# Performance work log

Hardware: AMD Instinct MI355X
Metric: run time of the kernel (lower is better)

Reference implementation:

```python
import jax, jax.numpy as jnp
import numpy as np
import math

# ---- dims ----
B, N, IN_DIM = 4, 512, 128
D, H, DH = 256, 8, 32          # embed_dim, heads, dim_head
L = 8                           # performer depth
M = int(DH * math.log(DH))      # 110 FAVOR+ random features (performer_pytorch default)
HID = 256                       # lstm hidden
FF = 4 * D
EPS_K = 1e-4                    # kernel feature eps
EPS_D = 1e-6                    # denominator eps


def setup_inputs() -> dict:
    key = jax.random.key(0)
    ks = iter(jax.random.split(key, 40))
    def nrm(shape, s=0.02):
        return jax.random.normal(next(ks), shape, dtype=jnp.float32) * s
    z = lambda shape: jnp.zeros(shape, jnp.float32)
    o = lambda shape: jnp.ones(shape, jnp.float32)
    return {
        "x": jax.random.normal(next(ks), (B, N, IN_DIM), dtype=jnp.float32),
        # input projection
        "Win_w": nrm((D, IN_DIM)), "Win_b": z((D,)),
        # performer layers (stacked over L)
        "ln1_w": o((L, D)), "ln1_b": z((L, D)),
        "Wq": nrm((L, D, D)), "bq": z((L, D)),
        "Wk": nrm((L, D, D)), "bk": z((L, D)),
        "Wv": nrm((L, D, D)), "bv": z((L, D)),
        "Wo": nrm((L, D, D)), "bo": z((L, D)),
        "proj": jax.random.normal(next(ks), (L, M, DH), dtype=jnp.float32),  # FAVOR+ projections
        "ln2_w": o((L, D)), "ln2_b": z((L, D)),
        "Wff1": nrm((L, FF, D)), "bff1": z((L, FF)),
        "Wff2": nrm((L, D, FF)), "bff2": z((L, D)),
        # BiLSTM: layer0 input D, layers1-2 input 2*HID; [dir] / [layer,dir] stacks
        "Wih0": nrm((2, 4 * HID, D)), "Whh0": nrm((2, 4 * HID, HID)), "b0": z((2, 2, 4 * HID)),
        "Wih12": nrm((2, 2, 4 * HID, 2 * HID)), "Whh12": nrm((2, 2, 4 * HID, HID)), "b12": z((2, 2, 2, 4 * HID)),
        # final head
        "fc_w": nrm((1, 2 * HID)), "fc_b": z((1,)),
    }


def layer_norm(x, w, b):
    mu = jnp.mean(x, -1, keepdims=True)
    var = jnp.mean((x - mu) ** 2, -1, keepdims=True)
    return (x - mu) * jax.lax.rsqrt(var + 1e-5) * w + b


def softmax_features(x, proj, is_query):
    # FAVOR+ positive softmax-kernel features. x:[b,h,n,dh], proj:[m,dh]
    xd = x * (DH ** -0.25)
    dd = jnp.einsum('bhnd,md->bhnm', xd, proj)
    diag = 0.5 * jnp.sum(xd * xd, -1)[..., None]            # [b,h,n,1]
    if is_query:
        stab = jnp.max(dd, axis=-1, keepdims=True)
    else:
        stab = jnp.max(dd, axis=(-2, -1), keepdims=True)
    return (M ** -0.5) * (jnp.exp(dd - diag - stab) + EPS_K)


def causal_linear_attention(qp, kp, v):
    # qp,kp:[b,h,n,m], v:[b,h,n,dv] -> [b,h,n,dv]; cumulative-sum causal form
    k_cum = jnp.cumsum(kp, axis=2)
    d_inv = 1.0 / (jnp.einsum('bhnm,bhnm->bhn', qp, k_cum) + EPS_D)
    ctx = jnp.cumsum(jnp.einsum('bhnm,bhnd->bhnmd', kp, v), axis=2)
    return jnp.einsum('bhnmd,bhnm,bhn->bhnd', ctx, qp, d_inv)


def performer_block(x, p):
    (lw1, lb1, wq, bq_, wk, bk_, wv, bv_, wo, bo_, pr, lw2, lb2, w1, b1, w2, b2) = p
    b, n = x.shape[0], x.shape[1]
    y = layer_norm(x, lw1, lb1)
    sh = lambda t: t.reshape(b, n, H, DH).transpose(0, 2, 1, 3)
    q = sh(y @ wq.T + bq_)
    k = sh(y @ wk.T + bk_)
    v = sh(y @ wv.T + bv_)
    qp = softmax_features(q, pr, True)
    kp = softmax_features(k, pr, False)
    o = causal_linear_attention(qp, kp, v)
    o = o.transpose(0, 2, 1, 3).reshape(b, n, D)
    x = x + o @ wo.T + bo_
    y = layer_norm(x, lw2, lb2)
    x = x + jax.nn.gelu(y @ w1.T + b1, approximate=False) @ w2.T + b2
    return x, None


def lstm_dir(x, wih, whh, b, reverse):
    # x:[B,N,in] -> hs:[B,N,HID]; torch gate order i,f,g,o
    xs = jnp.flip(x, 1) if reverse else x
    gi = xs.transpose(1, 0, 2) @ wih.T + b                  # [N,B,4H] precomputed input part
    def step(carry, g_in):
        h, c = carry
        g = g_in + h @ whh.T
        i, f, gg, oo = jnp.split(g, 4, axis=-1)
        c = jax.nn.sigmoid(f) * c + jax.nn.sigmoid(i) * jnp.tanh(gg)
        h = jax.nn.sigmoid(oo) * jnp.tanh(c)
        return (h, c), h
    h0 = jnp.zeros((x.shape[0], HID), x.dtype)
    _, hs = jax.lax.scan(step, (h0, h0), gi)
    hs = hs.transpose(1, 0, 2)
    return jnp.flip(hs, 1) if reverse else hs


def bilstm_layer(x, wih, whh, b):
    fwd = lstm_dir(x, wih[0], whh[0], b[0, 0] + b[0, 1], False)
    bwd = lstm_dir(x, wih[1], whh[1], b[1, 0] + b[1, 1], True)
    return jnp.concatenate([fwd, bwd], -1)


def reference(x, Win_w, Win_b, ln1_w, ln1_b, Wq, bq, Wk, bk, Wv, bv, Wo, bo, proj,
              ln2_w, ln2_b, Wff1, bff1, Wff2, bff2,
              Wih0, Whh0, b0, Wih12, Whh12, b12, fc_w, fc_b):
    h = x @ Win_w.T + Win_b
    params = (ln1_w, ln1_b, Wq, bq, Wk, bk, Wv, bv, Wo, bo, proj, ln2_w, ln2_b, Wff1, bff1, Wff2, bff2)
    h, _ = jax.lax.scan(performer_block, h, params)       # 8 performer layers
    # dropout is identity at eval
    h = bilstm_layer(h, Wih0, Whh0, b0)
    h = bilstm_layer(h, Wih12[0], Whh12[0], b12[0])
    h = bilstm_layer(h, Wih12[1], Whh12[1], b12[1])
    return h[:, -1, :] @ fc_w.T + fc_b                    # [B,1]
```

## Files before the change

### kernel.cpp

```cpp
#include <hip/hip_runtime.h>
#include <math.h>

#define B_    4
#define N_    512
#define D_    256
#define H_    8
#define DH_   32
#define M_    110
#define MP_   112
#define FF_   1024
#define HID_  256
#define ROWS_ 2048
#define CHUNK 32
#define NCH   16

#define OFF_H      0u
#define OFF_Y      524288u
#define OFF_Q      1048576u
#define OFF_K      1572864u
#define OFF_V      2097152u
#define OFF_O      2621440u
#define OFF_FF     3145728u
#define OFF_QP     5242880u
#define OFF_KP     7077888u
#define OFF_S      8912896u
#define OFF_MB     9437184u
#define OFF_P      10747904u
#define OFF_KSUM   12582912u
#define OFF_PK     12640256u
#define OFF_DIAG   12697600u
#define OFF_KMAX   12713984u

#define SCALE_X 0.42044820762685725f
#define SCALE_M 0.09534625892455924f

__device__ __forceinline__ float sigmoidf_(float x){ return 1.0f/(1.0f+expf(-x)); }
__device__ __forceinline__ float geluf_(float x){ return 0.5f*x*(1.0f+erff(x*0.70710678118654752f)); }
__device__ __forceinline__ unsigned encf_(float x){ unsigned u=__float_as_uint(x); return (u&0x80000000u)?~u:(u|0x80000000u); }
__device__ __forceinline__ float decf_(unsigned u){ return (u&0x80000000u)?__uint_as_float(u&0x7fffffffu):__uint_as_float(~u); }

typedef unsigned u32x4_ __attribute__((ext_vector_type(4)));

__device__ __forceinline__ u32x4_ ld4_far_(const unsigned* p){
  u32x4_ v;
  asm volatile("global_load_dwordx4 %0, %1, off sc0 sc1\n\ts_waitcnt vmcnt(0)"
               : "=v"(v) : "v"(p));
  return v;
}

__global__ __launch_bounds__(256) void gemm_k(
    const float* __restrict__ A, const float* __restrict__ W,
    const float* __restrict__ b1, const float* __restrict__ b2,
    const float* __restrict__ R, float* __restrict__ C,
    int M, int N, int K, int act)
{
  __shared__ float As[16][72];
  __shared__ float Ws[16][72];
  const int tid = threadIdx.x;
  const int tx = tid & 15, ty = tid >> 4;
  const int i0 = blockIdx.y * 64, j0 = blockIdx.x * 64;
  const int lr = tid >> 2, lc = (tid & 3) << 2;
  float acc[4][4] = {};
  for (int k0 = 0; k0 < K; k0 += 16) {
    float4 a4 = *(const float4*)(A + (size_t)(i0 + lr) * K + k0 + lc);
    float4 w4 = *(const float4*)(W + (size_t)(j0 + lr) * K + k0 + lc);
    __syncthreads();
    As[lc+0][lr]=a4.x; As[lc+1][lr]=a4.y; As[lc+2][lr]=a4.z; As[lc+3][lr]=a4.w;
    Ws[lc+0][lr]=w4.x; Ws[lc+1][lr]=w4.y; Ws[lc+2][lr]=w4.z; Ws[lc+3][lr]=w4.w;
    __syncthreads();
    #pragma unroll
    for (int kk = 0; kk < 16; kk++) {
      float4 av = *(const float4*)&As[kk][ty*4];
      float4 wv = *(const float4*)&Ws[kk][tx*4];
      acc[0][0] += av.x*wv.x; acc[0][1] += av.x*wv.y; acc[0][2] += av.x*wv.z; acc[0][3] += av.x*wv.w;
      acc[1][0] += av.y*wv.x; acc[1][1] += av.y*wv.y; acc[1][2] += av.y*wv.z; acc[1][3] += av.y*wv.w;
      acc[2][0] += av.z*wv.x; acc[2][1] += av.z*wv.y; acc[2][2] += av.z*wv.z; acc[2][3] += av.z*wv.w;
      acc[3][0] += av.w*wv.x; acc[3][1] += av.w*wv.y; acc[3][2] += av.w*wv.z; acc[3][3] += av.w*wv.w;
    }
  }
  #pragma unroll
  for (int ii = 0; ii < 4; ii++) {
    int gi_ = i0 + ty*4 + ii;
    #pragma unroll
    for (int jj = 0; jj < 4; jj++) {
      int gj = j0 + tx*4 + jj;
      float v = acc[ii][jj];
      if (b1) v += b1[gj];
      if (b2) v += b2[gj];
      if (act) v = geluf_(v);
      if (R) v += R[(size_t)gi_ * N + gj];
      C[(size_t)gi_ * N + gj] = v;
    }
  }
}

__global__ __launch_bounds__(256) void gemm3_k(
    const float* __restrict__ A,
    const float* __restrict__ W0, const float* __restrict__ W1, const float* __restrict__ W2,
    const float* __restrict__ c0_, const float* __restrict__ c1_, const float* __restrict__ c2_,
    float* __restrict__ O0, float* __restrict__ O1, float* __restrict__ O2)
{
  const int which = blockIdx.x >> 2;
  const float* W  = which == 0 ? W0 : which == 1 ? W1 : W2;
  const float* bb = which == 0 ? c0_ : which == 1 ? c1_ : c2_;
  float* C        = which == 0 ? O0 : which == 1 ? O1 : O2;
  __shared__ float As[16][72];
  __shared__ float Ws[16][72];
  const int tid = threadIdx.x;
  const int tx = tid & 15, ty = tid >> 4;
  const int i0 = blockIdx.y * 64, j0 = (blockIdx.x & 3) * 64;
  const int lr = tid >> 2, lc = (tid & 3) << 2;
  float acc[4][4] = {};
  for (int k0 = 0; k0 < 256; k0 += 16) {
    float4 a4 = *(const float4*)(A + (size_t)(i0 + lr) * 256 + k0 + lc);
    float4 w4 = *(const float4*)(W + (size_t)(j0 + lr) * 256 + k0 + lc);
    __syncthreads();
    As[lc+0][lr]=a4.x; As[lc+1][lr]=a4.y; As[lc+2][lr]=a4.z; As[lc+3][lr]=a4.w;
    Ws[lc+0][lr]=w4.x; Ws[lc+1][lr]=w4.y; Ws[lc+2][lr]=w4.z; Ws[lc+3][lr]=w4.w;
    __syncthreads();
    #pragma unroll
    for (int kk = 0; kk < 16; kk++) {
      float4 av = *(const float4*)&As[kk][ty*4];
      float4 wv = *(const float4*)&Ws[kk][tx*4];
      acc[0][0] += av.x*wv.x; acc[0][1] += av.x*wv.y; acc[0][2] += av.x*wv.z; acc[0][3] += av.x*wv.w;
      acc[1][0] += av.y*wv.x; acc[1][1] += av.y*wv.y; acc[1][2] += av.y*wv.z; acc[1][3] += av.y*wv.w;
      acc[2][0] += av.z*wv.x; acc[2][1] += av.z*wv.y; acc[2][2] += av.z*wv.z; acc[2][3] += av.z*wv.w;
      acc[3][0] += av.w*wv.x; acc[3][1] += av.w*wv.y; acc[3][2] += av.w*wv.z; acc[3][3] += av.w*wv.w;
    }
  }
  #pragma unroll
  for (int ii = 0; ii < 4; ii++) {
    int gi_ = i0 + ty*4 + ii;
    #pragma unroll
    for (int jj = 0; jj < 4; jj++) {
      int gj = j0 + tx*4 + jj;
      C[(size_t)gi_ * 256 + gj] = acc[ii][jj] + bb[gj];
    }
  }
}

__global__ __launch_bounds__(256) void gemmgi_k(
    const float* __restrict__ A, const float* __restrict__ W, const float* __restrict__ bvec,
    float* __restrict__ C, int K, int wGap, int bGap)
{
  const int dir = blockIdx.x >> 4;
  const float* Wd = W + (size_t)dir * wGap;
  const float* b1 = bvec + (size_t)dir * bGap;
  const float* b2 = b1 + 1024;
  float* Cd = C + (size_t)dir * 2097152;
  __shared__ float As[16][72];
  __shared__ float Ws[16][72];
  const int tid = threadIdx.x;
  const int tx = tid & 15, ty = tid >> 4;
  const int i0 = blockIdx.y * 64, j0 = (blockIdx.x & 15) * 64;
  const int lr = tid >> 2, lc = (tid & 3) << 2;
  float acc[4][4] = {};
  for (int k0 = 0; k0 < K; k0 += 16) {
    float4 a4 = *(const float4*)(A + (size_t)(i0 + lr) * K + k0 + lc);
    float4 w4 = *(const float4*)(Wd + (size_t)(j0 + lr) * K + k0 + lc);
    __syncthreads();
    As[lc+0][lr]=a4.x; As[lc+1][lr]=a4.y; As[lc+2][lr]=a4.z; As[lc+3][lr]=a4.w;
    Ws[lc+0][lr]=w4.x; Ws[lc+1][lr]=w4.y; Ws[lc+2][lr]=w4.z; Ws[lc+3][lr]=w4.w;
    __syncthreads();
    #pragma unroll
    for (int kk = 0; kk < 16; kk++) {
      float4 av = *(const float4*)&As[kk][ty*4];
      float4 wv = *(const float4*)&Ws[kk][tx*4];
      acc[0][0] += av.x*wv.x; acc[0][1] += av.x*wv.y; acc[0][2] += av.x*wv.z; acc[0][3] += av.x*wv.w;
      acc[1][0] += av.y*wv.x; acc[1][1] += av.y*wv.y; acc[1][2] += av.y*wv.z; acc[1][3] += av.y*wv.w;
      acc[2][0] += av.z*wv.x; acc[2][1] += av.z*wv.y; acc[2][2] += av.z*wv.z; acc[2][3] += av.z*wv.w;
      acc[3][0] += av.w*wv.x; acc[3][1] += av.w*wv.y; acc[3][2] += av.w*wv.z; acc[3][3] += av.w*wv.w;
    }
  }
  #pragma unroll
  for (int ii = 0; ii < 4; ii++) {
    int gi_ = i0 + ty*4 + ii;
    #pragma unroll
    for (int jj = 0; jj < 4; jj++) {
      int gj = j0 + tx*4 + jj;
      Cd[(size_t)gi_ * 1024 + gj] = acc[ii][jj] + b1[gj] + b2[gj];
    }
  }
}

__global__ __launch_bounds__(256) void ln_k(const float* __restrict__ x, const float* __restrict__ w,
                                            const float* __restrict__ b, float* __restrict__ y)
{
  const int row = blockIdx.x, t = threadIdx.x;
  float v = x[(size_t)row * 256 + t];
  float s = v;
  #pragma unroll
  for (int o = 32; o >= 1; o >>= 1) s += __shfl_xor(s, o, 64);
  __shared__ float w1_[4], w2_[4];
  const int wid = t >> 6, lane = t & 63;
  if (lane == 0) w1_[wid] = s;
  __syncthreads();
  float mu = (w1_[0] + w1_[1] + w1_[2] + w1_[3]) * (1.0f/256.0f);
  float d = v - mu;
  float s2 = d * d;
  #pragma unroll
  for (int o = 32; o >= 1; o >>= 1) s2 += __shfl_xor(s2, o, 64);
  if (lane == 0) w2_[wid] = s2;
  __syncthreads();
  float var = (w2_[0] + w2_[1] + w2_[2] + w2_[3]) * (1.0f/256.0f);
  y[(size_t)row * 256 + t] = d * (1.0f / sqrtf(var + 1e-5f)) * w[t] + b[t];
}

__global__ __launch_bounds__(256) void feat_k(const float* __restrict__ q, const float* __restrict__ kk,
                                              const float* __restrict__ proj,
                                              float* __restrict__ qp, float* __restrict__ kpraw,
                                              float* __restrict__ diagb, unsigned* __restrict__ kmax)
{
  const int isq = (blockIdx.x < 4096);
  const int bx = isq ? blockIdx.x : (blockIdx.x - 4096);
  const int wid = threadIdx.x >> 6, lane = threadIdx.x & 63;
  const int p = bx * 4 + wid;
  const int bh = p >> 9, n = p & 511;
  const int b = bh >> 3, h = bh & 7;
  __shared__ float xs[4][32];
  const float* xrow = (isq ? q : kk) + ((size_t)(b * N_ + n)) * D_ + h * DH_;
  if (lane < 32) xs[wid][lane] = xrow[lane] * SCALE_X;
  __syncthreads();
  float diag = 0.f;
  #pragma unroll
  for (int d = 0; d < 32; d++) { float xv = xs[wid][d]; diag += xv * xv; }
  diag *= 0.5f;
  const int m0 = lane, m1 = 64 + lane;
  float dd0 = 0.f, dd1 = -INFINITY;
  #pragma unroll
  for (int d = 0; d < 32; d++) dd0 += xs[wid][d] * proj[m0 * 32 + d];
  if (m1 < M_) {
    float a = 0.f;
    #pragma unroll
    for (int d = 0; d < 32; d++) a += xs[wid][d] * proj[m1 * 32 + d];
    dd1 = a;
  }
  float mx = fmaxf(dd0, dd1);
  #pragma unroll
  for (int o = 32; o >= 1; o >>= 1) mx = fmaxf(mx, __shfl_xor(mx, o, 64));
  if (isq) {
    float* out = qp + (size_t)p * MP_;
    out[m0] = SCALE_M * (expf(dd0 - diag - mx) + 1e-4f);
    if (m1 < M_)        out[m1] = SCALE_M * (expf(dd1 - diag - mx) + 1e-4f);
    else if (m1 < MP_)  out[m1] = 0.f;
  } else {
    float* out = kpraw + (size_t)p * MP_;
    out[m0] = dd0;
    if (m1 < M_) out[m1] = dd1;
    if (lane == 0) { diagb[p] = diag; atomicMax(kmax + bh, encf_(mx)); }
  }
}

__global__ __launch_bounds__(256) void csum_k(const float* __restrict__ kp, const float* __restrict__ v,
                                              const float* __restrict__ diagb, const unsigned* __restrict__ kmax,
                                              float* __restrict__ S, float* __restrict__ ksum)
{
  const int bh = blockIdx.x >> 4, c = blockIdx.x & 15;
  const int b = bh >> 3, h = bh & 7;
  __shared__ float kpc[CHUNK * MP_];
  __shared__ float vc[CHUNK][DH_];
  const float* kpbase = kp + ((size_t)bh * N_ + c * CHUNK) * MP_;
  const float kmx = decf_(kmax[bh]);
  const int r0 = bh * N_ + c * CHUNK;
  for (int f = threadIdx.x; f < CHUNK * MP_; f += 256) {
    int i = f / MP_, m = f - i * MP_;
    float raw = kpbase[f];
    float val = 0.f;
    if (m < M_) val = SCALE_M * (expf(raw - diagb[r0 + i] - kmx) + 1e-4f);
    kpc[f] = val;
  }
  for (int f = threadIdx.x; f < CHUNK * DH_; f += 256) {
    int i = f >> 5, d = f & 31;
    vc[i][d] = v[((size_t)(b * N_ + c * CHUNK + i)) * D_ + h * DH_ + d];
  }
  __syncthreads();
  const int d = threadIdx.x & 31, mg = threadIdx.x >> 5;
  float Sa[14] = {};
  for (int i = 0; i < CHUNK; i++) {
    float vv = vc[i][d];
    #pragma unroll
    for (int j = 0; j < 14; j++) Sa[j] += kpc[i * MP_ + mg * 14 + j] * vv;
  }
  float* Sout = S + (((size_t)blockIdx.x) * MP_ + mg * 14) * DH_ + d;
  #pragma unroll
  for (int j = 0; j < 14; j++) Sout[(size_t)j * DH_] = Sa[j];
  if (threadIdx.x < MP_) {
    float s = 0.f;
    for (int i = 0; i < CHUNK; i++) s += kpc[i * MP_ + threadIdx.x];
    ksum[(size_t)blockIdx.x * MP_ + threadIdx.x] = s;
  }
}

__global__ __launch_bounds__(256) void cpref_k(const float* __restrict__ S, const float* __restrict__ ksum,
                                               float* __restrict__ P, float* __restrict__ pk)
{
  const int bh = blockIdx.x;
  const int d = threadIdx.x & 31, mg = threadIdx.x >> 5;
  float run[14] = {};
  for (int c = 0; c < NCH; c++) {
    size_t base = (((size_t)(bh * NCH + c)) * MP_ + mg * 14) * DH_ + d;
    #pragma unroll
    for (int j = 0; j < 14; j++) { P[base + (size_t)j * DH_] = run[j]; run[j] += S[base + (size_t)j * DH_]; }
  }
  if (threadIdx.x < MP_) {
    float r = 0.f;
    for (int c = 0; c < NCH; c++) {
      size_t o = (size_t)(bh * NCH + c) * MP_ + threadIdx.x;
      pk[o] = r; r += ksum[o];
    }
  }
}

__global__ __launch_bounds__(256, 1) void attn_k(const float* __restrict__ qp, const float* __restrict__ kp,
                                                 const float* __restrict__ v, const float* __restrict__ P,
                                                 const float* __restrict__ pk,
                                                 const float* __restrict__ diagb, const unsigned* __restrict__ kmax,
                                                 float* __restrict__ o)
{
  const int bh = blockIdx.x >> 4, c = blockIdx.x & 15;
  const int b = bh >> 3, h = bh & 7;
  __shared__ float qpc[CHUNK * 113];
  __shared__ float kpc[CHUNK * 113];
  __shared__ float vc[CHUNK][DH_];
  __shared__ float Pl[MP_ * DH_];
  __shared__ float pkl[MP_];
  __shared__ float Al[CHUNK * 33];
  __shared__ float den[CHUNK];
  const int t = threadIdx.x;
  const float* qbase = qp + ((size_t)bh * N_ + c * CHUNK) * MP_;
  const float* kbase = kp + ((size_t)bh * N_ + c * CHUNK) * MP_;
  const float kmx = decf_(kmax[bh]);
  const int r0 = bh * N_ + c * CHUNK;
  for (int f = t; f < CHUNK * MP_; f += 256) {
    int i = f / MP_, m = f - i * MP_;
    qpc[i * 113 + m] = qbase[f];
    float raw = kbase[f];
    float val = 0.f;
    if (m < M_) val = SCALE_M * (expf(raw - diagb[r0 + i] - kmx) + 1e-4f);
    kpc[i * 113 + m] = val;
  }
  for (int f = t; f < CHUNK * DH_; f += 256) {
    int i = f >> 5, d = f & 31;
    vc[i][d] = v[((size_t)(b * N_ + c * CHUNK + i)) * D_ + h * DH_ + d];
  }
  for (int f = t; f < MP_ * DH_; f += 256) Pl[f] = P[((size_t)blockIdx.x) * MP_ * DH_ + f];
  if (t < MP_) pkl[t] = pk[(size_t)blockIdx.x * MP_ + t];
  __syncthreads();
  {
    const int ti = t >> 4, tj = t & 15;
    float a00 = 0.f, a01 = 0.f, a10 = 0.f, a11 = 0.f;
    for (int m = 0; m < MP_; m++) {
      float q0 = qpc[(ti*2+0)*113 + m], q1 = qpc[(ti*2+1)*113 + m];
      float k0 = kpc[(tj*2+0)*113 + m], k1 = kpc[(tj*2+1)*113 + m];
      a00 += q0*k0; a01 += q0*k1; a10 += q1*k0; a11 += q1*k1;
    }
    const int i0_ = ti*2, j0_ = tj*2;
    Al[(i0_  )*33 + j0_  ] = (j0_   <= i0_  ) ? a00 : 0.f;
    Al[(i0_  )*33 + j0_+1] = (j0_+1 <= i0_  ) ? a01 : 0.f;
    Al[(i0_+1)*33 + j0_  ] = (j0_   <= i0_+1) ? a10 : 0.f;
    Al[(i0_+1)*33 + j0_+1] = (j0_+1 <= i0_+1) ? a11 : 0.f;
  }
  __syncthreads();
  if (t < CHUNK) {
    const int i = t; float s = 0.f;
    for (int m = 0; m < MP_; m++) s += qpc[i*113 + m] * pkl[m];
    for (int j = 0; j <= i; j++) s += Al[i*33 + j];
    den[i] = 1.0f / (s + 1e-6f);
  }
  __syncthreads();
  {
    const int d = t & 31, ig = t >> 5;
    float Pd[MP_];
    #pragma unroll
    for (int m = 0; m < MP_; m++) Pd[m] = Pl[m * DH_ + d];
    float vd[CHUNK];
    #pragma unroll
    for (int j = 0; j < CHUNK; j++) vd[j] = vc[j][d];
    for (int r = 0; r < 4; r++) {
      const int i = ig * 4 + r;
      float acc = 0.f;
      #pragma unroll
      for (int m = 0; m < MP_; m++) acc += qpc[i*113 + m] * Pd[m];
      #pragma unroll
      for (int j = 0; j < CHUNK; j++) acc += Al[i*33 + j] * vd[j];
      o[((size_t)(b * N_ + c * CHUNK + i)) * D_ + h * DH_ + d] = acc * den[i];
    }
  }
}

__global__ __launch_bounds__(256, 1) void rec_k(
    const float* __restrict__ gi, const float* __restrict__ whh,
    float* __restrict__ hs, float* __restrict__ hx)
{
  const int bid = blockIdx.x;
  if ((bid & 7) > 1) return;
  const int dir = bid & 7;
  const int s = bid >> 3;
  if (s >= 16) return;
  const int t = threadIdx.x;

  __shared__ __align__(16) float h_sh[4][256];
  __shared__ __align__(16) float red[64 * 33];

  __builtin_amdgcn_fence(__ATOMIC_ACQUIRE, "agent");

  const float* giD = gi + (size_t)dir * 2097152;
  const float* whD = whh + (size_t)dir * 262144;
  float* hxD = hx + (size_t)dir * 524288;

  const int rg = t & 31, kq = t >> 5;
  float4 w4[2][8];
  #pragma unroll
  for (int rr = 0; rr < 2; rr++) {
    const int rho = rg * 2 + rr;
    const int grow = (rho >> 4) * 256 + s * 16 + (rho & 15);
    const float4* src = (const float4*)(whD + (size_t)grow * 256 + kq * 32);
    #pragma unroll
    for (int q = 0; q < 8; q++) w4[rr][q] = src[q];
  }

  const int j = t & 15, bb = t >> 4;
  const float* pgi0 = giD + (size_t)bb * 524288 + (size_t)(s * 16 + j);

  ((float4*)h_sh)[t] = make_float4(0.f, 0.f, 0.f, 0.f);
  float c0 = 0.f;
  __syncthreads();

  int n = dir ? 511 : 0;
  float gnext[4];
  if (t < 64) {
    #pragma unroll
    for (int g = 0; g < 4; g++) gnext[g] = pgi0[(size_t)n * 1024 + g * 256];
  }

  for (int step = 0; step < 512; step++) {
    const int n2 = dir ? (510 - step) : (step + 1);
    float gcur[4];
    if (t < 64) {
      #pragma unroll
      for (int g = 0; g < 4; g++) gcur[g] = gnext[g];
      if (step < 511) {
        #pragma unroll
        for (int g = 0; g < 4; g++) gnext[g] = pgi0[(size_t)n2 * 1024 + g * 256];
      }
    }

    float acc[2][4] = {};
    #pragma unroll
    for (int q = 0; q < 8; q++) {
      float4 h0 = *(const float4*)&h_sh[0][kq * 32 + q * 4];
      float4 h1 = *(const float4*)&h_sh[1][kq * 32 + q * 4];
      float4 h2 = *(const float4*)&h_sh[2][kq * 32 + q * 4];
      float4 h3 = *(const float4*)&h_sh[3][kq * 32 + q * 4];
      #pragma unroll
      for (int rr = 0; rr < 2; rr++) {
        float4 w = w4[rr][q];
        acc[rr][0] += w.x*h0.x + w.y*h0.y + w.z*h0.z + w.w*h0.w;
        acc[rr][1] += w.x*h1.x + w.y*h1.y + w.z*h1.z + w.w*h1.w;
        acc[rr][2] += w.x*h2.x + w.y*h2.y + w.z*h2.z + w.w*h2.w;
        acc[rr][3] += w.x*h3.x + w.y*h3.y + w.z*h3.z + w.w*h3.w;
      }
    }
    #pragma unroll
    for (int rr = 0; rr < 2; rr++)
      #pragma unroll
      for (int b = 0; b < 4; b++)
        red[(rg * 2 + rr) * 33 + b * 8 + kq] = acc[rr][b];
    __syncthreads();

    if (t < 64) {
      float pre[4];
      #pragma unroll
      for (int g = 0; g < 4; g++) {
        const float* rp = &red[(g * 16 + j) * 33 + bb * 8];
        float sum = gcur[g];
        #pragma unroll
        for (int q = 0; q < 8; q++) sum += rp[q];
        pre[g] = sum;
      }
      c0 = sigmoidf_(pre[1]) * c0 + sigmoidf_(pre[0]) * tanhf(pre[2]);
      const float hv = sigmoidf_(pre[3]) * tanhf(c0);
      if (step < 511) {
        __hip_atomic_store(hxD + (size_t)step * 1024 + bb * 256 + s * 16 + j, hv,
                           __ATOMIC_RELAXED, __HIP_MEMORY_SCOPE_AGENT);
      }
      hs[(size_t)(bb * 512 + n) * 512 + dir * 256 + s * 16 + j] = hv;
    }

    if (step < 511) {
      const unsigned* pp = (const unsigned*)(hxD + (size_t)step * 1024) + t * 4;
      u32x4_ v = ld4_far_(pp);
      while (v.x == 0xFFFFFFFFu || v.y == 0xFFFFFFFFu ||
             v.z == 0xFFFFFFFFu || v.w == 0xFFFFFFFFu) {
        v = ld4_far_(pp);
      }
      float4 hv4;
      hv4.x = __uint_as_float(v.x); hv4.y = __uint_as_float(v.y);
      hv4.z = __uint_as_float(v.z); hv4.w = __uint_as_float(v.w);
      ((float4*)h_sh)[t] = hv4;
      __syncthreads();
    }
    n = n2;
  }
}

__global__ __launch_bounds__(256) void fc_k(const float* __restrict__ hs, const float* __restrict__ fw,
                                            const float* __restrict__ fb, float* __restrict__ out)
{
  const int t = threadIdx.x;
  float p[4] = {};
  for (int j = t; j < 512; j += 256) {
    const float w = fw[j];
    #pragma unroll
    for (int b = 0; b < 4; b++) p[b] += hs[(size_t)(b * 512 + 511) * 512 + j] * w;
  }
  #pragma unroll
  for (int b = 0; b < 4; b++)
    #pragma unroll
    for (int o = 32; o >= 1; o >>= 1) p[b] += __shfl_xor(p[b], o, 64);
  __shared__ float r4[4][4];
  const int wid = t >> 6, lane = t & 63;
  if (lane == 0) {
    #pragma unroll
    for (int b = 0; b < 4; b++) r4[b][wid] = p[b];
  }
  __syncthreads();
  if (t == 0) {
    #pragma unroll
    for (int b = 0; b < 4; b++) out[b] = r4[b][0] + r4[b][1] + r4[b][2] + r4[b][3] + fb[0];
  }
}

extern "C" void kernel_launch(void* const* d_in, const int* in_sizes, int n_in,
                              void* d_out, int out_size, void* d_ws, size_t ws_size,
                              hipStream_t stream) {
  (void)in_sizes; (void)n_in; (void)out_size; (void)ws_size;
  const float* x     = (const float*)d_in[0];
  const float* Win_w = (const float*)d_in[1];
  const float* Win_b = (const float*)d_in[2];
  const float* ln1w  = (const float*)d_in[3];
  const float* ln1b  = (const float*)d_in[4];
  const float* Wq    = (const float*)d_in[5];
  const float* bq    = (const float*)d_in[6];
  const float* Wk    = (const float*)d_in[7];
  const float* bk    = (const float*)d_in[8];
  const float* Wv    = (const float*)d_in[9];
  const float* bv    = (const float*)d_in[10];
  const float* Wo    = (const float*)d_in[11];
  const float* bo    = (const float*)d_in[12];
  const float* proj  = (const float*)d_in[13];
  const float* ln2w  = (const float*)d_in[14];
  const float* ln2b  = (const float*)d_in[15];
  const float* Wff1  = (const float*)d_in[16];
  const float* bff1  = (const float*)d_in[17];
  const float* Wff2  = (const float*)d_in[18];
  const float* bff2  = (const float*)d_in[19];
  const float* Wih0  = (const float*)d_in[20];
  const float* Whh0  = (const float*)d_in[21];
  const float* b0    = (const float*)d_in[22];
  const float* Wih12 = (const float*)d_in[23];
  const float* Whh12 = (const float*)d_in[24];
  const float* b12   = (const float*)d_in[25];
  const float* fcw   = (const float*)d_in[26];
  const float* fcb   = (const float*)d_in[27];

  float* ws = (float*)d_ws;
  float* H   = ws + OFF_H;
  float* Y   = ws + OFF_Y;
  float* Q   = ws + OFF_Q;
  float* Kb  = ws + OFF_K;
  float* V   = ws + OFF_V;
  float* O   = ws + OFF_O;
  float* FFb = ws + OFF_FF;
  float* QP  = ws + OFF_QP;
  float* KP  = ws + OFF_KP;
  float* S   = ws + OFF_S;
  float* P   = ws + OFF_P;
  float* KS  = ws + OFF_KSUM;
  float* PK  = ws + OFF_PK;
  float* DG  = ws + OFF_DIAG;
  unsigned* KMAX = (unsigned*)(ws + OFF_KMAX);
  float* GI  = ws + OFF_QP;
  float* MA  = ws + OFF_MB;
  float* BLa = ws + OFF_FF;
  float* BLb = ws + OFF_FF + 1048576;

  const dim3 blk(256);
  const dim3 g256(4, 32);
  const dim3 g768(12, 32);
  const dim3 g1024(16, 32);
  const dim3 g2048(32, 32);

  gemm_k<<<g256, blk, 0, stream>>>(x, Win_w, Win_b, nullptr, nullptr, H, ROWS_, 256, 128, 0);

  for (int l = 0; l < 8; l++) {
    const float* prj = proj + (size_t)l * 3520;
    ln_k<<<ROWS_, blk, 0, stream>>>(H, ln1w + l*256, ln1b + l*256, Y);
    gemm3_k<<<g768, blk, 0, stream>>>(Y, Wq + (size_t)l*65536, Wk + (size_t)l*65536, Wv + (size_t)l*65536,
                                      bq + l*256, bk + l*256, bv + l*256, Q, Kb, V);
    (void)hipMemsetAsync(KMAX, 0, 32 * sizeof(unsigned), stream);
    feat_k<<<8192, blk, 0, stream>>>(Q, Kb, prj, QP, KP, DG, KMAX);
    csum_k<<<512, blk, 0, stream>>>(KP, V, DG, KMAX, S, KS);
    cpref_k<<<32, blk, 0, stream>>>(S, KS, P, PK);
    attn_k<<<512, blk, 0, stream>>>(QP, KP, V, P, PK, DG, KMAX, O);
    gemm_k<<<g256, blk, 0, stream>>>(O, Wo + (size_t)l*65536, bo + l*256, nullptr, H, H, ROWS_, 256, 256, 0);
    ln_k<<<ROWS_, blk, 0, stream>>>(H, ln2w + l*256, ln2b + l*256, Y);
    gemm_k<<<g1024, blk, 0, stream>>>(Y, Wff1 + (size_t)l*262144, bff1 + l*1024, nullptr, nullptr, FFb, ROWS_, 1024, 256, 1);
    gemm_k<<<g256, blk, 0, stream>>>(FFb, Wff2 + (size_t)l*262144, bff2 + l*256, nullptr, H, H, ROWS_, 256, 1024, 0);
  }

  (void)hipMemsetAsync(MA, 0xFF, 3145728u * sizeof(float), stream);

  gemmgi_k<<<g2048, blk, 0, stream>>>(H, Wih0, b0, GI, 256, 262144, 2048);
  rec_k<<<128, blk, 0, stream>>>(GI, Whh0, BLa, MA);

  gemmgi_k<<<g2048, blk, 0, stream>>>(BLa, Wih12, b12, GI, 512, 524288, 2048);
  rec_k<<<128, blk, 0, stream>>>(GI, Whh12, BLb, MA + 1048576);

  gemmgi_k<<<g2048, blk, 0, stream>>>(BLb, Wih12 + 1048576, b12 + 4096, GI, 512, 524288, 2048);
  rec_k<<<128, blk, 0, stream>>>(GI, Whh12 + 524288, BLa, MA + 2097152);

  fc_k<<<1, blk, 0, stream>>>(BLa, fcw, fcb, (float*)d_out);
}
```

Baseline: 6.807 ms.

## Use 32x32 GEMM tiles for narrow outputs, prefetch tiles, fold prefix into attention

Adds a 32x32-tile GEMM with 2x2 register blocking for the 256-wide output GEMMs (input projection, Wo, FF2) and the QKV GEMM, giving four times as many blocks to fill the GPU. All tiled GEMMs now load the next K-slice into registers while the current shared-memory tile is being computed. The separate chunk-prefix kernel is removed: each attention block sums the preceding chunk states itself, which repeats some global reads. The per-layer KMAX memset is replaced by a single memset over per-layer slices, saving one launch per layer.

```diff
diff --git a/kernel.cpp b/kernel.cpp
--- a/kernel.cpp
+++ b/kernel.cpp
@@ -48,6 +48,111 @@
   return v;
 }
 
+__global__ __launch_bounds__(256) void gemms_k(
+    const float* __restrict__ A, const float* __restrict__ W,
+    const float* __restrict__ b1, const float* __restrict__ b2,
+    const float* __restrict__ R, float* __restrict__ C,
+    int M, int N, int K, int act)
+{
+  __shared__ float As[16][36];
+  __shared__ float Ws[16][36];
+  const int tid = threadIdx.x;
+  const int tx = tid & 15, ty = tid >> 4;
+  const int i0 = blockIdx.y * 32, j0 = blockIdx.x * 32;
+  const int lr = tid >> 3, lc = (tid & 7) << 1;
+  const float* pA = A + (size_t)(i0 + lr) * K + lc;
+  const float* pW = W + (size_t)(j0 + lr) * K + lc;
+  float a00=0.f, a01=0.f, a10=0.f, a11=0.f;
+  float2 a2 = *(const float2*)pA;
+  float2 w2 = *(const float2*)pW;
+  for (int k0 = 0; k0 < K; k0 += 16) {
+    __syncthreads();
+    As[lc+0][lr]=a2.x; As[lc+1][lr]=a2.y;
+    Ws[lc+0][lr]=w2.x; Ws[lc+1][lr]=w2.y;
+    float2 a2n = a2, w2n = w2;
+    if (k0 + 16 < K) {
+      a2n = *(const float2*)(pA + k0 + 16);
+      w2n = *(const float2*)(pW + k0 + 16);
+    }
+    __syncthreads();
+    #pragma unroll
+    for (int kk = 0; kk < 16; kk++) {
+      float2 av = *(const float2*)&As[kk][ty*2];
+      float2 wv = *(const float2*)&Ws[kk][tx*2];
+      a00 += av.x*wv.x; a01 += av.x*wv.y;
+      a10 += av.y*wv.x; a11 += av.y*wv.y;
+    }
+    a2 = a2n; w2 = w2n;
+  }
+  float accv[2][2] = {{a00,a01},{a10,a11}};
+  #pragma unroll
+  for (int ii = 0; ii < 2; ii++) {
+    int gi_ = i0 + ty*2 + ii;
+    #pragma unroll
+    for (int jj = 0; jj < 2; jj++) {
+      int gj = j0 + tx*2 + jj;
+      float v = accv[ii][jj];
+      if (b1) v += b1[gj];
+      if (b2) v += b2[gj];
+      if (act) v = geluf_(v);
+      if (R) v += R[(size_t)gi_ * N + gj];
+      C[(size_t)gi_ * N + gj] = v;
+    }
+  }
+}
+
+__global__ __launch_bounds__(256) void gemm3_k(
+    const float* __restrict__ A,
+    const float* __restrict__ W0, const float* __restrict__ W1, const float* __restrict__ W2,
+    const float* __restrict__ c0_, const float* __restrict__ c1_, const float* __restrict__ c2_,
+    float* __restrict__ O0, float* __restrict__ O1, float* __restrict__ O2)
+{
+  const int which = blockIdx.x >> 3;
+  const float* W  = which == 0 ? W0 : which == 1 ? W1 : W2;
+  const float* bb = which == 0 ? c0_ : which == 1 ? c1_ : c2_;
+  float* C        = which == 0 ? O0 : which == 1 ? O1 : O2;
+  __shared__ float As[16][36];
+  __shared__ float Ws[16][36];
+  const int tid = threadIdx.x;
+  const int tx = tid & 15, ty = tid >> 4;
+  const int i0 = blockIdx.y * 32, j0 = (blockIdx.x & 7) * 32;
+  const int lr = tid >> 3, lc = (tid & 7) << 1;
+  const float* pA = A + (size_t)(i0 + lr) * 256 + lc;
+  const float* pW = W + (size_t)(j0 + lr) * 256 + lc;
+  float a00=0.f, a01=0.f, a10=0.f, a11=0.f;
+  float2 a2 = *(const float2*)pA;
+  float2 w2 = *(const float2*)pW;
+  for (int k0 = 0; k0 < 256; k0 += 16) {
+    __syncthreads();
+    As[lc+0][lr]=a2.x; As[lc+1][lr]=a2.y;
+    Ws[lc+0][lr]=w2.x; Ws[lc+1][lr]=w2.y;
+    float2 a2n = a2, w2n = w2;
+    if (k0 + 16 < 256) {
+      a2n = *(const float2*)(pA + k0 + 16);
+      w2n = *(const float2*)(pW + k0 + 16);
+    }
+    __syncthreads();
+    #pragma unroll
+    for (int kk = 0; kk < 16; kk++) {
+      float2 av = *(const float2*)&As[kk][ty*2];
+      float2 wv = *(const float2*)&Ws[kk][tx*2];
+      a00 += av.x*wv.x; a01 += av.x*wv.y;
+      a10 += av.y*wv.x; a11 += av.y*wv.y;
+    }
+    a2 = a2n; w2 = w2n;
+  }
+  float accv[2][2] = {{a00,a01},{a10,a11}};
+  #pragma unroll
+  for (int ii = 0; ii < 2; ii++) {
+    int gi_ = i0 + ty*2 + ii;
+    #pragma unroll
+    for (int jj = 0; jj < 2; jj++) {
+      int gj = j0 + tx*2 + jj;
+      C[(size_t)gi_ * 256 + gj] = accv[ii][jj] + bb[gj];
+    }
+  }
+}
+
 __global__ __launch_bounds__(256) void gemm_k(
     const float* __restrict__ A, const float* __restrict__ W,
     const float* __restrict__ b1, const float* __restrict__ b2,
@@ -60,13 +165,20 @@
   const int tx = tid & 15, ty = tid >> 4;
   const int i0 = blockIdx.y * 64, j0 = blockIdx.x * 64;
   const int lr = tid >> 2, lc = (tid & 3) << 2;
+  const float* pA = A + (size_t)(i0 + lr) * K + lc;
+  const float* pW = W + (size_t)(j0 + lr) * K + lc;
   float acc[4][4] = {};
+  float4 a4 = *(const float4*)pA;
+  float4 w4 = *(const float4*)pW;
   for (int k0 = 0; k0 < K; k0 += 16) {
-    float4 a4 = *(const float4*)(A + (size_t)(i0 + lr) * K + k0 + lc);
-    float4 w4 = *(const float4*)(W + (size_t)(j0 + lr) * K + k0 + lc);
     __syncthreads();
     As[lc+0][lr]=a4.x; As[lc+1][lr]=a4.y; As[lc+2][lr]=a4.z; As[lc+3][lr]=a4.w;
     Ws[lc+0][lr]=w4.x; Ws[lc+1][lr]=w4.y; Ws[lc+2][lr]=w4.z; Ws[lc+3][lr]=w4.w;
+    float4 a4n = a4, w4n = w4;
+    if (k0 + 16 < K) {
+      a4n = *(const float4*)(pA + k0 + 16);
+      w4n = *(const float4*)(pW + k0 + 16);
+    }
     __syncthreads();
     #pragma unroll
     for (int kk = 0; kk < 16; kk++) {
@@ -77,6 +189,7 @@
       acc[2][0] += av.z*wv.x; acc[2][1] += av.z*wv.y; acc[2][2] += av.z*wv.z; acc[2][3] += av.z*wv.w;
       acc[3][0] += av.w*wv.x; acc[3][1] += av.w*wv.y; acc[3][2] += av.w*wv.z; acc[3][3] += av.w*wv.w;
     }
+    a4 = a4n; w4 = w4n;
   }
   #pragma unroll
   for (int ii = 0; ii < 4; ii++) {
@@ -90,51 +203,6 @@
       if (act) v = geluf_(v);
       if (R) v += R[(size_t)gi_ * N + gj];
       C[(size_t)gi_ * N + gj] = v;
-    }
-  }
-}
-
-__global__ __launch_bounds__(256) void gemm3_k(
-    const float* __restrict__ A,
-    const float* __restrict__ W0, const float* __restrict__ W1, const float* __restrict__ W2,
-    const float* __restrict__ c0_, const float* __restrict__ c1_, const float* __restrict__ c2_,
-    float* __restrict__ O0, float* __restrict__ O1, float* __restrict__ O2)
-{
-  const int which = blockIdx.x >> 2;
-  const float* W  = which == 0 ? W0 : which == 1 ? W1 : W2;
-  const float* bb = which == 0 ? c0_ : which == 1 ? c1_ : c2_;
-  float* C        = which == 0 ? O0 : which == 1 ? O1 : O2;
-  __shared__ float As[16][72];
-  __shared__ float Ws[16][72];
-  const int tid = threadIdx.x;
-  const int tx = tid & 15, ty = tid >> 4;
-  const int i0 = blockIdx.y * 64, j0 = (blockIdx.x & 3) * 64;
-  const int lr = tid >> 2, lc = (tid & 3) << 2;
-  float acc[4][4] = {};
-  for (int k0 = 0; k0 < 256; k0 += 16) {
-    float4 a4 = *(const float4*)(A + (size_t)(i0 + lr) * 256 + k0 + lc);
-    float4 w4 = *(const float4*)(W + (size_t)(j0 + lr) * 256 + k0 + lc);
-    __syncthreads();
-    As[lc+0][lr]=a4.x; As[lc+1][lr]=a4.y; As[lc+2][lr]=a4.z; As[lc+3][lr]=a4.w;
-    Ws[lc+0][lr]=w4.x; Ws[lc+1][lr]=w4.y; Ws[lc+2][lr]=w4.z; Ws[lc+3][lr]=w4.w;
-    __syncthreads();
-    #pragma unroll
-    for (int kk = 0; kk < 16; kk++) {
-      float4 av = *(const float4*)&As[kk][ty*4];
-      float4 wv = *(const float4*)&Ws[kk][tx*4];
-      acc[0][0] += av.x*wv.x; acc[0][1] += av.x*wv.y; acc[0][2] += av.x*wv.z; acc[0][3] += av.x*wv.w;
-      acc[1][0] += av.y*wv.x; acc[1][1] += av.y*wv.y; acc[1][2] += av.y*wv.z; acc[1][3] += av.y*wv.w;
-      acc[2][0] += av.z*wv.x; acc[2][1] += av.z*wv.y; acc[2][2] += av.z*wv.z; acc[2][3] += av.z*wv.w;
-      acc[3][0] += av.w*wv.x; acc[3][1] += av.w*wv.y; acc[3][2] += av.w*wv.z; acc[3][3] += av.w*wv.w;
-    }
-  }
-  #pragma unroll
-  for (int ii = 0; ii < 4; ii++) {
-    int gi_ = i0 + ty*4 + ii;
-    #pragma unroll
-    for (int jj = 0; jj < 4; jj++) {
-      int gj = j0 + tx*4 + jj;
-      C[(size_t)gi_ * 256 + gj] = acc[ii][jj] + bb[gj];
     }
   }
 }
@@ -154,13 +222,20 @@
   const int tx = tid & 15, ty = tid >> 4;
   const int i0 = blockIdx.y * 64, j0 = (blockIdx.x & 15) * 64;
   const int lr = tid >> 2, lc = (tid & 3) << 2;
+  const float* pA = A + (size_t)(i0 + lr) * K + lc;
+  const float* pW = Wd + (size_t)(j0 + lr) * K + lc;
   float acc[4][4] = {};
+  float4 a4 = *(const float4*)pA;
+  float4 w4 = *(const float4*)pW;
   for (int k0 = 0; k0 < K; k0 += 16) {
-    float4 a4 = *(const float4*)(A + (size_t)(i0 + lr) * K + k0 + lc);
-    float4 w4 = *(const float4*)(Wd + (size_t)(j0 + lr) * K + k0 + lc);
     __syncthreads();
     As[lc+0][lr]=a4.x; As[lc+1][lr]=a4.y; As[lc+2][lr]=a4.z; As[lc+3][lr]=a4.w;
     Ws[lc+0][lr]=w4.x; Ws[lc+1][lr]=w4.y; Ws[lc+2][lr]=w4.z; Ws[lc+3][lr]=w4.w;
+    float4 a4n = a4, w4n = w4;
+    if (k0 + 16 < K) {
+      a4n = *(const float4*)(pA + k0 + 16);
+      w4n = *(const float4*)(pW + k0 + 16);
+    }
     __syncthreads();
     #pragma unroll
     for (int kk = 0; kk < 16; kk++) {
@@ -171,6 +246,7 @@
       acc[2][0] += av.z*wv.x; acc[2][1] += av.z*wv.y; acc[2][2] += av.z*wv.z; acc[2][3] += av.z*wv.w;
       acc[3][0] += av.w*wv.x; acc[3][1] += av.w*wv.y; acc[3][2] += av.w*wv.z; acc[3][3] += av.w*wv.w;
     }
+    a4 = a4n; w4 = w4n;
   }
   #pragma unroll
   for (int ii = 0; ii < 4; ii++) {
@@ -291,29 +367,9 @@
   }
 }
 
-__global__ __launch_bounds__(256) void cpref_k(const float* __restrict__ S, const float* __restrict__ ksum,
-                                               float* __restrict__ P, float* __restrict__ pk)
-{
-  const int bh = blockIdx.x;
-  const int d = threadIdx.x & 31, mg = threadIdx.x >> 5;
-  float run[14] = {};
-  for (int c = 0; c < NCH; c++) {
-    size_t base = (((size_t)(bh * NCH + c)) * MP_ + mg * 14) * DH_ + d;
-    #pragma unroll
-    for (int j = 0; j < 14; j++) { P[base + (size_t)j * DH_] = run[j]; run[j] += S[base + (size_t)j * DH_]; }
-  }
-  if (threadIdx.x < MP_) {
-    float r = 0.f;
-    for (int c = 0; c < NCH; c++) {
-      size_t o = (size_t)(bh * NCH + c) * MP_ + threadIdx.x;
-      pk[o] = r; r += ksum[o];
-    }
-  }
-}
-
 __global__ __launch_bounds__(256, 1) void attn_k(const float* __restrict__ qp, const float* __restrict__ kp,
-                                                 const float* __restrict__ v, const float* __restrict__ P,
-                                                 const float* __restrict__ pk,
+                                                 const float* __restrict__ v,
+                                                 const float* __restrict__ S, const float* __restrict__ ksum,
                                                  const float* __restrict__ diagb, const unsigned* __restrict__ kmax,
                                                  float* __restrict__ o)
 {
@@ -343,8 +399,20 @@
     int i = f >> 5, d = f & 31;
     vc[i][d] = v[((size_t)(b * N_ + c * CHUNK + i)) * D_ + h * DH_ + d];
   }
-  for (int f = t; f < MP_ * DH_; f += 256) Pl[f] = P[((size_t)blockIdx.x) * MP_ * DH_ + f];
-  if (t < MP_) pkl[t] = pk[(size_t)blockIdx.x * MP_ + t];
+  {
+    const float* Sb = S + (size_t)(bh * NCH) * MP_ * DH_;
+    for (int f = t; f < MP_ * DH_; f += 256) {
+      float accp = 0.f;
+      for (int cc = 0; cc < c; cc++) accp += Sb[(size_t)cc * MP_ * DH_ + f];
+      Pl[f] = accp;
+    }
+    if (t < MP_) {
+      const float* Kb2 = ksum + (size_t)(bh * NCH) * MP_;
+      float r = 0.f;
+      for (int cc = 0; cc < c; cc++) r += Kb2[(size_t)cc * MP_ + t];
+      pkl[t] = r;
+    }
+  }
   __syncthreads();
   {
     const int ti = t >> 4, tj = t & 15;
@@ -575,9 +643,7 @@
   float* QP  = ws + OFF_QP;
   float* KP  = ws + OFF_KP;
   float* S   = ws + OFF_S;
-  float* P   = ws + OFF_P;
   float* KS  = ws + OFF_KSUM;
-  float* PK  = ws + OFF_PK;
   float* DG  = ws + OFF_DIAG;
   unsigned* KMAX = (unsigned*)(ws + OFF_KMAX);
   float* GI  = ws + OFF_QP;
@@ -586,38 +652,39 @@
   float* BLb = ws + OFF_FF + 1048576;
 
   const dim3 blk(256);
-  const dim3 g256(4, 32);
-  const dim3 g768(12, 32);
+  const dim3 gs256(8, 64);
+  const dim3 g3(24, 64);
   const dim3 g1024(16, 32);
-  const dim3 g2048(32, 32);
-
-  gemm_k<<<g256, blk, 0, stream>>>(x, Win_w, Win_b, nullptr, nullptr, H, ROWS_, 256, 128, 0);
+  const dim3 ggi(32, 32);
+
+  (void)hipMemsetAsync(KMAX, 0, 256 * sizeof(unsigned), stream);
+
+  gemms_k<<<gs256, blk, 0, stream>>>(x, Win_w, Win_b, nullptr, nullptr, H, ROWS_, 256, 128, 0);
 
   for (int l = 0; l < 8; l++) {
     const float* prj = proj + (size_t)l * 3520;
+    unsigned* kmx = KMAX + l * 32;
     ln_k<<<ROWS_, blk, 0, stream>>>(H, ln1w + l*256, ln1b + l*256, Y);
-    gemm3_k<<<g768, blk, 0, stream>>>(Y, Wq + (size_t)l*65536, Wk + (size_t)l*65536, Wv + (size_t)l*65536,
-                                      bq + l*256, bk + l*256, bv + l*256, Q, Kb, V);
-    (void)hipMemsetAsync(KMAX, 0, 32 * sizeof(unsigned), stream);
-    feat_k<<<8192, blk, 0, stream>>>(Q, Kb, prj, QP, KP, DG, KMAX);
-    csum_k<<<512, blk, 0, stream>>>(KP, V, DG, KMAX, S, KS);
-    cpref_k<<<32, blk, 0, stream>>>(S, KS, P, PK);
-    attn_k<<<512, blk, 0, stream>>>(QP, KP, V, P, PK, DG, KMAX, O);
-    gemm_k<<<g256, blk, 0, stream>>>(O, Wo + (size_t)l*65536, bo + l*256, nullptr, H, H, ROWS_, 256, 256, 0);
+    gemm3_k<<<g3, blk, 0, stream>>>(Y, Wq + (size_t)l*65536, Wk + (size_t)l*65536, Wv + (size_t)l*65536,
+                                    bq + l*256, bk + l*256, bv + l*256, Q, Kb, V);
+    feat_k<<<8192, blk, 0, stream>>>(Q, Kb, prj, QP, KP, DG, kmx);
+    csum_k<<<512, blk, 0, stream>>>(KP, V, DG, kmx, S, KS);
+    attn_k<<<512, blk, 0, stream>>>(QP, KP, V, S, KS, DG, kmx, O);
+    gemms_k<<<gs256, blk, 0, stream>>>(O, Wo + (size_t)l*65536, bo + l*256, nullptr, H, H, ROWS_, 256, 256, 0);
     ln_k<<<ROWS_, blk, 0, stream>>>(H, ln2w + l*256, ln2b + l*256, Y);
     gemm_k<<<g1024, blk, 0, stream>>>(Y, Wff1 + (size_t)l*262144, bff1 + l*1024, nullptr, nullptr, FFb, ROWS_, 1024, 256, 1);
-    gemm_k<<<g256, blk, 0, stream>>>(FFb, Wff2 + (size_t)l*262144, bff2 + l*256, nullptr, H, H, ROWS_, 256, 1024, 0);
+    gemms_k<<<gs256, blk, 0, stream>>>(FFb, Wff2 + (size_t)l*262144, bff2 + l*256, nullptr, H, H, ROWS_, 256, 1024, 0);
   }
 
   (void)hipMemsetAsync(MA, 0xFF, 3145728u * sizeof(float), stream);
 
-  gemmgi_k<<<g2048, blk, 0, stream>>>(H, Wih0, b0, GI, 256, 262144, 2048);
+  gemmgi_k<<<ggi, blk, 0, stream>>>(H, Wih0, b0, GI, 256, 262144, 2048);
   rec_k<<<128, blk, 0, stream>>>(GI, Whh0, BLa, MA);
 
-  gemmgi_k<<<g2048, blk, 0, stream>>>(BLa, Wih12, b12, GI, 512, 524288, 2048);
+  gemmgi_k<<<ggi, blk, 0, stream>>>(BLa, Wih12, b12, GI, 512, 524288, 2048);
   rec_k<<<128, blk, 0, stream>>>(GI, Whh12, BLb, MA + 1048576);
 
-  gemmgi_k<<<g2048, blk, 0, stream>>>(BLb, Wih12 + 1048576, b12 + 4096, GI, 512, 524288, 2048);
+  gemmgi_k<<<ggi, blk, 0, stream>>>(BLb, Wih12 + 1048576, b12 + 4096, GI, 512, 524288, 2048);
   rec_k<<<128, blk, 0, stream>>>(GI, Whh12 + 524288, BLa, MA + 2097152);
 
   fc_k<<<1, blk, 0, stream>>>(BLa, fcw, fcb, (float*)d_out);
```

New measurement: 7.293 ms. 7.1% more time.
